# Kernel tuning notes

Hardware: AMD Instinct MI355X
Metric: run time of the kernel (lower is better)

The kernel has to match this reference:

```python
import jax, jax.numpy as jnp
import numpy as np

N = 8192       # nodes
IN_F = 512     # in_features
OUT_F = 256    # out_features


def setup_inputs() -> dict:
    key = jax.random.key(0)
    k1, k2, k3, k4 = jax.random.split(key, 4)
    # xavier_uniform-like scales for params
    w_scale = 1.414 * (6.0 / (IN_F + OUT_F)) ** 0.5
    a_scale = 1.414 * (6.0 / (2 * OUT_F + 1)) ** 0.5
    x = jax.random.normal(k1, (N, IN_F), jnp.float32)
    W = jax.random.uniform(k2, (IN_F, OUT_F), jnp.float32, -w_scale, w_scale)
    a = jax.random.uniform(k3, (2 * OUT_F, 1), jnp.float32, -a_scale, a_scale)
    adj = jax.random.randint(k4, (N, N), 0, 2, jnp.int32)
    return {"x": x, "W": W, "a": a, "adj": adj}


def reference(x, W, a, adj):
    # h = x @ W : [N, OUT_F]
    h = x @ W
    f = W.shape[1]
    a1, a2 = a[:f], a[f:]          # each [OUT_F, 1]
    # Original builds a_input[i,j] = concat(h_i, h_j) then matmuls with a.
    # Equivalent decomposition: e[i,j] = h_i . a1 + h_j . a2
    e = (h @ a1) + (h @ a2).T      # [N, N]
    neg = jnp.float32(-9e15)
    attention = jnp.where(adj > 0, e, neg)   # no softmax in the original
    h_prime = attention @ h        # [N, OUT_F]
    return h_prime
```

## Files before the change

### kernel.cpp

```cpp
#include <hip/hip_runtime.h>


#define NEG_BIG (-9000000000000000.0f)
#define POS_BIG (9000000000000000.0f)

typedef __bf16 bf16x8 __attribute__((ext_vector_type(8)));
typedef float f32x16 __attribute__((ext_vector_type(16)));

static __device__ __forceinline__ unsigned short f2bf(float f) {
  unsigned u = __builtin_bit_cast(unsigned, f);
  u = u + 0x7FFFu + ((u >> 16) & 1u);
  return (unsigned short)(u >> 16);
}
static __device__ __forceinline__ float bfbits2f(unsigned hi16) {
  return __builtin_bit_cast(float, hi16 << 16);
}
static __device__ __forceinline__ unsigned pk2(float a, float b) {
  return (unsigned)f2bf(a) | ((unsigned)f2bf(b) << 16);
}
static __device__ __forceinline__ unsigned m2(int a, int b) {
  return (unsigned)(a + (b << 16)) * 0x3F80u;
}
static __device__ __forceinline__ bf16x8 asbf(int4 q) {
  return __builtin_bit_cast(bf16x8, q);
}
static __device__ __forceinline__ f32x16 mfma(bf16x8 a, int4 b, f32x16 c) {
  return __builtin_amdgcn_mfma_f32_32x32x16_bf16(a, asbf(b), c, 0, 0, 0);
}

__global__ void k1a_wt(const float* __restrict__ W, unsigned short* __restrict__ WT,
                       float* __restrict__ T) {
  const int i = blockIdx.x * 256 + threadIdx.x;
  const int k = i >> 8, n = i & 255;
  WT[n * 512 + k] = f2bf(W[i]);
  if (blockIdx.x == 0) T[threadIdx.x] = 0.f;
}

__global__ __launch_bounds__(256) void k1b_h(const float* __restrict__ x,
    const unsigned short* __restrict__ WT, unsigned short* __restrict__ hP) {
  const int t = threadIdx.x;
  const int w = t >> 6, l = t & 63, l31 = l & 31, lh = l >> 5;
  const int gw = blockIdx.x * 4 + w;
  const int mt = gw >> 3, nt = gw & 7;
  const int m0 = mt << 5, n0 = nt << 5;
  f32x16 acc;
  for (int i = 0; i < 16; ++i) acc[i] = 0.f;
  const float* xr = x + (size_t)(m0 + l31) * 512 + lh * 8;
  const unsigned short* wr = WT + (size_t)(n0 + l31) * 512 + lh * 8;
#pragma unroll 4
  for (int k0 = 0; k0 < 512; k0 += 16) {
    float4 xa = *(const float4*)(xr + k0);
    float4 xb = *(const float4*)(xr + k0 + 4);
    int4 wb = *(const int4*)(wr + k0);
    union { unsigned u[4]; bf16x8 v; } A;
    A.u[0] = pk2(xa.x, xa.y); A.u[1] = pk2(xa.z, xa.w);
    A.u[2] = pk2(xb.x, xb.y); A.u[3] = pk2(xb.z, xb.w);
    acc = __builtin_amdgcn_mfma_f32_32x32x16_bf16(A.v, asbf(wb), acc, 0, 0, 0);
  }
#pragma unroll
  for (int reg = 0; reg < 16; ++reg) {
    const int m = m0 + (reg & 3) + 8 * (reg >> 2) + 4 * lh;
    const int n = n0 + l31;
    hP[(size_t)(m >> 5) * 8192 + n * 32 + (m & 31)] = f2bf(acc[reg]);
  }
}

__global__ __launch_bounds__(256) void k2_colsum(const unsigned short* __restrict__ hP,
                                                 float* __restrict__ T) {
  const int t = threadIdx.x;
  const int b = blockIdx.x;
  const int4* p = (const int4*)(hP + (size_t)b * 8192 + t * 32);
  int4 q0 = p[0], q1 = p[1], q2 = p[2], q3 = p[3];
  float s = 0.f;
  const unsigned* u0 = (const unsigned*)&q0;
  const unsigned* u1 = (const unsigned*)&q1;
  const unsigned* u2 = (const unsigned*)&q2;
  const unsigned* u3 = (const unsigned*)&q3;
#pragma unroll
  for (int i = 0; i < 4; ++i) {
    s += bfbits2f(u0[i] & 0xFFFFu) + bfbits2f(u0[i] >> 16);
    s += bfbits2f(u1[i] & 0xFFFFu) + bfbits2f(u1[i] >> 16);
    s += bfbits2f(u2[i] & 0xFFFFu) + bfbits2f(u2[i] >> 16);
    s += bfbits2f(u3[i] & 0xFFFFu) + bfbits2f(u3[i] >> 16);
  }
  atomicAdd(&T[t], s);
}

__global__ void k2b_init(const float* __restrict__ T, float* __restrict__ out) {
  const int i = blockIdx.x * 256 + threadIdx.x;
  const int n4 = (i & 63) * 4;
  float4 tv = *(const float4*)(T + n4);
  float4 o;
  o.x = NEG_BIG * tv.x; o.y = NEG_BIG * tv.y;
  o.z = NEG_BIG * tv.z; o.w = NEG_BIG * tv.w;
  ((float4*)out)[i] = o;
}

#define LSTR 68
__global__ __launch_bounds__(256, 4) void k3_att(const int* __restrict__ adj,
    const unsigned short* __restrict__ hP, float* __restrict__ out) {
  __shared__ unsigned short A[2][64 * LSTR];
  const int t = threadIdx.x;
  const int blk = blockIdx.x;
  const int s = blk & 7;
  const int rt = blk >> 3;
  const int w = t >> 6;
  const int l = t & 63;
  const int l31 = l & 31;
  const int lh = l >> 5;
  const int n0 = w << 6;

  const int srow = t >> 4;
  const int scol = (t & 15) << 2;
  const int* aBase = adj + (size_t)(rt * 64 + srow) * 8192 + s * 1024 + scol;
  unsigned short* const wA0 = &A[0][srow * LSTR + scol];
  unsigned short* const wA1 = &A[1][srow * LSTR + scol];

  const int fr0 = l31 * (LSTR * 2) + lh * 16;
  const int fr1 = fr0 + 32 * (LSTR * 2);

  const unsigned short* hB = hP + (n0 + l31) * 32 + lh * 8;

  f32x16 a00, a01, a10, a11;
  for (int i = 0; i < 16; ++i) { a00[i] = 0.f; a01[i] = 0.f; a10[i] = 0.f; a11[i] = 0.f; }

  {
    int4 v0 = *(const int4*)(aBase);
    int4 v1 = *(const int4*)(aBase + (size_t)16 * 8192);
    int4 v2 = *(const int4*)(aBase + (size_t)32 * 8192);
    int4 v3 = *(const int4*)(aBase + (size_t)48 * 8192);
    *(uint2*)(wA0)             = make_uint2(m2(v0.x, v0.y), m2(v0.z, v0.w));
    *(uint2*)(wA0 + 16 * LSTR) = make_uint2(m2(v1.x, v1.y), m2(v1.z, v1.w));
    *(uint2*)(wA0 + 32 * LSTR) = make_uint2(m2(v2.x, v2.y), m2(v2.z, v2.w));
    *(uint2*)(wA0 + 48 * LSTR) = make_uint2(m2(v3.x, v3.y), m2(v3.z, v3.w));
  }

  for (int it = 0; it < 16; ++it) {
    __syncthreads();
    int4 v0, v1, v2, v3;
    if (it < 15) {
      const int* ab = aBase + (it + 1) * 64;
      v0 = *(const int4*)(ab);
      v1 = *(const int4*)(ab + (size_t)16 * 8192);
      v2 = *(const int4*)(ab + (size_t)32 * 8192);
      v3 = *(const int4*)(ab + (size_t)48 * 8192);
    }
    const unsigned short* hb0 = hB + (size_t)(s * 32 + it * 2) * 8192;
    const unsigned short* hb1 = hb0 + 8192;
    int4 b00 = *(const int4*)(hb0);
    int4 b01 = *(const int4*)(hb0 + 16);
    int4 b0n = *(const int4*)(hb0 + 1024);
    int4 b1n = *(const int4*)(hb0 + 1040);
    int4 b20 = *(const int4*)(hb1);
    int4 b21 = *(const int4*)(hb1 + 16);
    int4 b2n = *(const int4*)(hb1 + 1024);
    int4 b3n = *(const int4*)(hb1 + 1040);

    const char* Ab = (const char*)&A[it & 1][0];
#pragma unroll
    for (int ks = 0; ks < 4; ++ks) {
      bf16x8 A0 = *(const bf16x8*)(Ab + fr0 + ks * 32);
      bf16x8 A1 = *(const bf16x8*)(Ab + fr1 + ks * 32);
      int4 Bn0 = (ks == 0) ? b00 : (ks == 1) ? b01 : (ks == 2) ? b20 : b21;
      int4 Bn1 = (ks == 0) ? b0n : (ks == 1) ? b1n : (ks == 2) ? b2n : b3n;
      a00 = mfma(A0, Bn0, a00);
      a01 = mfma(A0, Bn1, a01);
      a10 = mfma(A1, Bn0, a10);
      a11 = mfma(A1, Bn1, a11);
    }
    if (it < 15) {
      unsigned short* wn = ((it & 1) ? wA0 : wA1);
      *(uint2*)(wn)             = make_uint2(m2(v0.x, v0.y), m2(v0.z, v0.w));
      *(uint2*)(wn + 16 * LSTR) = make_uint2(m2(v1.x, v1.y), m2(v1.z, v1.w));
      *(uint2*)(wn + 32 * LSTR) = make_uint2(m2(v2.x, v2.y), m2(v2.z, v2.w));
      *(uint2*)(wn + 48 * LSTR) = make_uint2(m2(v3.x, v3.y), m2(v3.z, v3.w));
    }
  }

  const int rb0 = rt * 64 + 4 * lh;
  const int nn = n0 + l31;
#pragma unroll
  for (int reg = 0; reg < 16; ++reg) {
    const int ro = (reg & 3) + 8 * (reg >> 2);
    float* p = out + (size_t)(rb0 + ro) * 256 + nn;
    atomicAdd(p, POS_BIG * a00[reg]);
    atomicAdd(p + 32, POS_BIG * a01[reg]);
    float* p2 = p + 32 * 256;
    atomicAdd(p2, POS_BIG * a10[reg]);
    atomicAdd(p2 + 32, POS_BIG * a11[reg]);
  }
}

extern "C" void kernel_launch(void* const* d_in, const int* in_sizes, int n_in,
                              void* d_out, int out_size, void* d_ws, size_t ws_size,
                              hipStream_t stream) {
  const float* x = (const float*)d_in[0];
  const float* W = (const float*)d_in[1];
  const int* adj = (const int*)d_in[3];
  float* out = (float*)d_out;
  char* ws = (char*)d_ws;
  unsigned short* WT = (unsigned short*)(ws);
  unsigned short* hP = (unsigned short*)(ws + (1 << 20));
  float* T = (float*)(ws + (6 << 20));

  k1a_wt<<<512, 256, 0, stream>>>(W, WT, T);
  k1b_h<<<512, 256, 0, stream>>>(x, WT, hP);
  k2_colsum<<<256, 256, 0, stream>>>(hP, T);
  k2b_init<<<2048, 256, 0, stream>>>(T, out);
  k3_att<<<1024, 256, 0, stream>>>(adj, hP, out);
}
```

Baseline: 476.8 us.

## Retile attention matmul per-wave and replace atomics with split-K partial buffer reduction

Each wave now owns a 32-row adjacency tile across all 256 output columns (8 accumulators), with per-wave LDS double buffering and no block-wide barriers, and it prefetches two adjacency stages ahead. The final float atomics into out are replaced, when workspace allows, by plain stores into 8 split-K partial buffers that a separate kernel sums and combines with the column-sum term. The aim is to remove atomic contention and barrier stalls. The cost is 64 MB of extra partial-buffer traffic, more register pressure (launch bounds 2), and every wave reloading all h B-fragments.

```diff
diff --git a/kernel.cpp b/kernel.cpp
--- a/kernel.cpp
+++ b/kernel.cpp
@@ -96,99 +96,109 @@
   ((float4*)out)[i] = o;
 }
 
-#define LSTR 68
-__global__ __launch_bounds__(256, 4) void k3_att(const int* __restrict__ adj,
-    const unsigned short* __restrict__ hP, float* __restrict__ out) {
-  __shared__ unsigned short A[2][64 * LSTR];
+#define A_LSTR 68
+template<int MODE>
+__global__ __launch_bounds__(256, 2) void k3_att(const int* __restrict__ adj,
+    const unsigned short* __restrict__ hP, float* __restrict__ outp) {
+  __shared__ unsigned short S[4][2][32 * A_LSTR];
   const int t = threadIdx.x;
   const int blk = blockIdx.x;
   const int s = blk & 7;
-  const int rt = blk >> 3;
+  const int g = blk >> 3;
   const int w = t >> 6;
+  const int rtile = g * 4 + w;
   const int l = t & 63;
-  const int l31 = l & 31;
-  const int lh = l >> 5;
-  const int n0 = w << 6;
-
-  const int srow = t >> 4;
-  const int scol = (t & 15) << 2;
-  const int* aBase = adj + (size_t)(rt * 64 + srow) * 8192 + s * 1024 + scol;
-  unsigned short* const wA0 = &A[0][srow * LSTR + scol];
-  unsigned short* const wA1 = &A[1][srow * LSTR + scol];
-
-  const int fr0 = l31 * (LSTR * 2) + lh * 16;
-  const int fr1 = fr0 + 32 * (LSTR * 2);
-
-  const unsigned short* hB = hP + (n0 + l31) * 32 + lh * 8;
-
-  f32x16 a00, a01, a10, a11;
-  for (int i = 0; i < 16; ++i) { a00[i] = 0.f; a01[i] = 0.f; a10[i] = 0.f; a11[i] = 0.f; }
-
-  {
-    int4 v0 = *(const int4*)(aBase);
-    int4 v1 = *(const int4*)(aBase + (size_t)16 * 8192);
-    int4 v2 = *(const int4*)(aBase + (size_t)32 * 8192);
-    int4 v3 = *(const int4*)(aBase + (size_t)48 * 8192);
-    *(uint2*)(wA0)             = make_uint2(m2(v0.x, v0.y), m2(v0.z, v0.w));
-    *(uint2*)(wA0 + 16 * LSTR) = make_uint2(m2(v1.x, v1.y), m2(v1.z, v1.w));
-    *(uint2*)(wA0 + 32 * LSTR) = make_uint2(m2(v2.x, v2.y), m2(v2.z, v2.w));
-    *(uint2*)(wA0 + 48 * LSTR) = make_uint2(m2(v3.x, v3.y), m2(v3.z, v3.w));
-  }
-
-  for (int it = 0; it < 16; ++it) {
-    __syncthreads();
-    int4 v0, v1, v2, v3;
-    if (it < 15) {
-      const int* ab = aBase + (it + 1) * 64;
-      v0 = *(const int4*)(ab);
-      v1 = *(const int4*)(ab + (size_t)16 * 8192);
-      v2 = *(const int4*)(ab + (size_t)32 * 8192);
-      v3 = *(const int4*)(ab + (size_t)48 * 8192);
+  const int l31 = l & 31, lh = l >> 5;
+  const int R0 = rtile * 32;
+
+  const int sr = l >> 4;
+  const int sc = (l & 15) << 2;
+  const int* aB = adj + (size_t)(R0 + sr) * 8192 + s * 1024 + sc;
+  unsigned short* const S0 = &S[w][0][0];
+  unsigned short* const S1 = &S[w][1][0];
+  const int woff = sr * A_LSTR + sc;
+
+  f32x16 acc[8];
+#pragma unroll
+  for (int nt = 0; nt < 8; ++nt)
+#pragma unroll
+    for (int i = 0; i < 16; ++i) acc[nt][i] = 0.f;
+
+#define LOADS(dst, it)                                                     \
+  _Pragma("unroll")                                                        \
+  for (int q = 0; q < 8; ++q)                                              \
+    dst[q] = *(const int4*)(aB + (size_t)q * 4 * 8192 + (it) * 64);
+#define PACKW(buf, src)                                                    \
+  _Pragma("unroll")                                                        \
+  for (int q = 0; q < 8; ++q)                                              \
+    *(uint2*)(buf + woff + q * 4 * A_LSTR) =                               \
+        make_uint2(m2(src[q].x, src[q].y), m2(src[q].z, src[q].w));
+
+  int4 gA[8], gB[8];
+  LOADS(gA, 0)
+  LOADS(gB, 1)
+  PACKW(S0, gA)
+
+  const unsigned short* hW = hP + (size_t)s * 32 * 8192 + (size_t)l31 * 32 + lh * 8;
+
+#define COMPUTE(it, buf)                                                   \
+  {                                                                        \
+    const unsigned short* hB = hW + (size_t)(it) * 2 * 8192;               \
+    _Pragma("unroll")                                                      \
+    for (int ks = 0; ks < 4; ++ks) {                                       \
+      const bf16x8 Af =                                                    \
+          *(const bf16x8*)(buf + l31 * A_LSTR + ks * 16 + lh * 8);         \
+      const unsigned short* hk = hB + (ks >> 1) * 8192 + (ks & 1) * 16;    \
+      _Pragma("unroll")                                                    \
+      for (int nt = 0; nt < 8; ++nt) {                                     \
+        int4 bq = *(const int4*)(hk + nt * 1024);                          \
+        acc[nt] = mfma(Af, bq, acc[nt]);                                   \
+      }                                                                    \
+    }                                                                      \
+  }
+
+#pragma unroll 1
+  for (int it = 0; it < 16; it += 2) {
+    if (it + 2 < 16) { LOADS(gA, it + 2) }
+    PACKW(S1, gB)
+    COMPUTE(it, S0)
+    if (it + 3 < 16) { LOADS(gB, it + 3) }
+    if (it + 2 < 16) { PACKW(S0, gA) }
+    COMPUTE(it + 1, S1)
+  }
+
+#pragma unroll
+  for (int nt = 0; nt < 8; ++nt) {
+    const int nn = nt * 32 + l31;
+#pragma unroll
+    for (int reg = 0; reg < 16; ++reg) {
+      const int rr = R0 + (reg & 3) + 8 * (reg >> 2) + 4 * lh;
+      if (MODE == 0) {
+        outp[(size_t)s * 2097152 + (size_t)rr * 256 + nn] = acc[nt][reg];
+      } else {
+        atomicAdd(outp + (size_t)rr * 256 + nn, POS_BIG * acc[nt][reg]);
+      }
     }
-    const unsigned short* hb0 = hB + (size_t)(s * 32 + it * 2) * 8192;
-    const unsigned short* hb1 = hb0 + 8192;
-    int4 b00 = *(const int4*)(hb0);
-    int4 b01 = *(const int4*)(hb0 + 16);
-    int4 b0n = *(const int4*)(hb0 + 1024);
-    int4 b1n = *(const int4*)(hb0 + 1040);
-    int4 b20 = *(const int4*)(hb1);
-    int4 b21 = *(const int4*)(hb1 + 16);
-    int4 b2n = *(const int4*)(hb1 + 1024);
-    int4 b3n = *(const int4*)(hb1 + 1040);
-
-    const char* Ab = (const char*)&A[it & 1][0];
-#pragma unroll
-    for (int ks = 0; ks < 4; ++ks) {
-      bf16x8 A0 = *(const bf16x8*)(Ab + fr0 + ks * 32);
-      bf16x8 A1 = *(const bf16x8*)(Ab + fr1 + ks * 32);
-      int4 Bn0 = (ks == 0) ? b00 : (ks == 1) ? b01 : (ks == 2) ? b20 : b21;
-      int4 Bn1 = (ks == 0) ? b0n : (ks == 1) ? b1n : (ks == 2) ? b2n : b3n;
-      a00 = mfma(A0, Bn0, a00);
-      a01 = mfma(A0, Bn1, a01);
-      a10 = mfma(A1, Bn0, a10);
-      a11 = mfma(A1, Bn1, a11);
-    }
-    if (it < 15) {
-      unsigned short* wn = ((it & 1) ? wA0 : wA1);
-      *(uint2*)(wn)             = make_uint2(m2(v0.x, v0.y), m2(v0.z, v0.w));
-      *(uint2*)(wn + 16 * LSTR) = make_uint2(m2(v1.x, v1.y), m2(v1.z, v1.w));
-      *(uint2*)(wn + 32 * LSTR) = make_uint2(m2(v2.x, v2.y), m2(v2.z, v2.w));
-      *(uint2*)(wn + 48 * LSTR) = make_uint2(m2(v3.x, v3.y), m2(v3.z, v3.w));
-    }
-  }
-
-  const int rb0 = rt * 64 + 4 * lh;
-  const int nn = n0 + l31;
-#pragma unroll
-  for (int reg = 0; reg < 16; ++reg) {
-    const int ro = (reg & 3) + 8 * (reg >> 2);
-    float* p = out + (size_t)(rb0 + ro) * 256 + nn;
-    atomicAdd(p, POS_BIG * a00[reg]);
-    atomicAdd(p + 32, POS_BIG * a01[reg]);
-    float* p2 = p + 32 * 256;
-    atomicAdd(p2, POS_BIG * a10[reg]);
-    atomicAdd(p2 + 32, POS_BIG * a11[reg]);
-  }
+  }
+}
+
+__global__ __launch_bounds__(256) void k4_reduce(const float* __restrict__ P,
+    const float* __restrict__ T, float* __restrict__ out) {
+  const int i = blockIdx.x * 256 + threadIdx.x;
+  float4 tv = *(const float4*)(T + (i & 63) * 4);
+  const float4* P4 = (const float4*)P;
+  float sx = 0.f, sy = 0.f, sz = 0.f, sw = 0.f;
+#pragma unroll
+  for (int sp = 0; sp < 8; ++sp) {
+    float4 v = P4[(size_t)sp * 524288 + i];
+    sx += v.x; sy += v.y; sz += v.z; sw += v.w;
+  }
+  float4 o;
+  o.x = POS_BIG * sx + NEG_BIG * tv.x;
+  o.y = POS_BIG * sy + NEG_BIG * tv.y;
+  o.z = POS_BIG * sz + NEG_BIG * tv.z;
+  o.w = POS_BIG * sw + NEG_BIG * tv.w;
+  ((float4*)out)[i] = o;
 }
 
 extern "C" void kernel_launch(void* const* d_in, const int* in_sizes, int n_in,
@@ -202,10 +212,18 @@
   unsigned short* WT = (unsigned short*)(ws);
   unsigned short* hP = (unsigned short*)(ws + (1 << 20));
   float* T = (float*)(ws + (6 << 20));
+  float* P = (float*)(ws + (8 << 20));
+
+  const bool fit = ws_size >= ((size_t)(8 << 20) + (size_t)64 * 1024 * 1024);
 
   k1a_wt<<<512, 256, 0, stream>>>(W, WT, T);
   k1b_h<<<512, 256, 0, stream>>>(x, WT, hP);
   k2_colsum<<<256, 256, 0, stream>>>(hP, T);
-  k2b_init<<<2048, 256, 0, stream>>>(T, out);
-  k3_att<<<1024, 256, 0, stream>>>(adj, hP, out);
-}
+  if (fit) {
+    k3_att<0><<<512, 256, 0, stream>>>(adj, hP, P);
+    k4_reduce<<<2048, 256, 0, stream>>>(P, T, out);
+  } else {
+    k2b_init<<<2048, 256, 0, stream>>>(T, out);
+    k3_att<1><<<512, 256, 0, stream>>>(adj, hP, out);
+  }
+}
```

Result: no change. 485.8 us (+1.9%).
